# Performance work log

Hardware: AMD Instinct MI355X
Metric: run time of the kernel (lower is better)

Reference implementation:

```python
import jax, jax.numpy as jnp
import numpy as np

V, E, H, LE, B, T = 32001, 512, 512, 512, 128, 512
EPS = 1e-5


def setup_inputs() -> dict:
    key = jax.random.key(0)
    ks = jax.random.split(key, 12)
    s = 0.02
    return {
        "label": jax.random.randint(ks[0], (B, T), 0, V, dtype=jnp.int64) if jax.config.jax_enable_x64 else jax.random.randint(ks[0], (B, T), 0, V, dtype=jnp.int32),
        "label_len": jax.random.randint(ks[1], (B,), 0, T, dtype=jnp.int32),
        "embed_w": jax.random.normal(ks[2], (V, E), jnp.float32) * s,
        "i2h_w": jax.random.normal(ks[3], (5 * H, E), jnp.float32) * s,
        "i2h_b": jax.random.normal(ks[4], (5 * H,), jnp.float32) * s,
        "h2h_w": jax.random.normal(ks[5], (5 * H, H), jnp.float32) * s,
        "h2h_b": jax.random.normal(ks[6], (5 * H,), jnp.float32) * s,
        "lin0_w": jax.random.normal(ks[7], (LE, H), jnp.float32) * s,
        "lin0_b": jax.random.normal(ks[8], (LE,), jnp.float32) * s,
        "bn0_g": jnp.ones((LE,), jnp.float32),
        "bn0_b": jnp.zeros((LE,), jnp.float32),
        "lin1_w": jax.random.normal(ks[9], (LE, LE), jnp.float32) * s,
        "lin1_b": jax.random.normal(ks[10], (LE,), jnp.float32) * s,
        "bn1_g": jnp.ones((LE,), jnp.float32),
        "bn1_b": jnp.zeros((LE,), jnp.float32),
    }


def _batchnorm(x, g, b):
    # BatchNorm1d in training mode: biased batch statistics over batch dim
    m = jnp.mean(x, axis=0)
    v = jnp.mean((x - m) ** 2, axis=0)
    return (x - m) * jax.lax.rsqrt(v + EPS) * g + b


def reference(label, label_len, embed_w, i2h_w, i2h_b, h2h_w, h2h_b,
              lin0_w, lin0_b, bn0_g, bn0_b, lin1_w, lin1_b, bn1_g, bn1_b):
    xt = embed_w[label]                                   # [B,T,E]
    pre = jnp.einsum('bte,ge->btg', xt, i2h_w) + i2h_b    # precomputed i2h, [B,T,5H]
    pre = pre.transpose(1, 0, 2)                          # [T,B,5H]

    def step(carry, p_t):
        h, c = carry
        s = p_t + h @ h2h_w.T + h2h_b                     # [B,5H]
        sig = jax.nn.sigmoid(s[:, :3 * H])
        in_g, f_g, out_g = sig[:, :H], sig[:, H:2 * H], sig[:, 2 * H:3 * H]
        in_t = jnp.maximum(s[:, 3 * H:4 * H], s[:, 4 * H:5 * H])  # maxout transform
        nc = f_g * c + in_g * in_t
        nh = out_g * jnp.tanh(nc)
        return (nh, nc), nh

    h0 = jnp.zeros((B, H), pre.dtype)
    _, outs = jax.lax.scan(step, (h0, h0), pre)           # outs: [T,B,H]

    # pick output at timestep label_len[i] for each sample
    x = outs[label_len, jnp.arange(B)]                    # [B,H]

    x = _batchnorm(x @ lin0_w.T + lin0_b, bn0_g, bn0_b)
    x = jax.nn.relu(x)                                    # dropout identity (eval)
    x = _batchnorm(x @ lin1_w.T + lin1_b, bn1_g, bn1_b)
    return x
```

## Files before the change

kernel.cpp:

```cpp
#include <hip/hip_runtime.h>

typedef _Float16 h16x8 __attribute__((ext_vector_type(8)));
typedef _Float16 h16x4 __attribute__((ext_vector_type(4)));
typedef float fx4 __attribute__((ext_vector_type(4)));
typedef unsigned int u32x4 __attribute__((ext_vector_type(4)));
typedef unsigned long long ull;

#define PRE_S 2560.0f
#define PRE_INV (1.0f / 2560.0f)

__global__ __launch_bounds__(256) void f2h_kernel(const float* __restrict__ src,
                                                  _Float16* __restrict__ dst,
                                                  int n4) {
  int i = blockIdx.x * 256 + threadIdx.x;
  if (i < n4) {
    float4 v = ((const float4*)src)[i];
    h16x4 o = {(_Float16)v.x, (_Float16)v.y, (_Float16)v.z, (_Float16)v.w};
    *(h16x4*)&dst[i * 4] = o;
  }
}

__global__ __launch_bounds__(256) void gemm1_kernel(
    const int* __restrict__ label, const int* __restrict__ label_len,
    const float* __restrict__ embed_w,
    const _Float16* __restrict__ Bh,
    signed char* __restrict__ pre8) {
  const int bx = blockIdx.x;
  const int by = blockIdx.y;
  const int bidx = by >> 2;
  const int t0 = (by & 3) * 128;
  if (t0 > label_len[bidx]) return;

  const int tid = threadIdx.x;
  const int lane = tid & 63;
  const int wv = tid >> 6;
  const int wm = (wv & 1) * 64;
  const int wn = (wv >> 1) * 64;

  __shared__ _Float16 As[128 * 40];
  __shared__ _Float16 Bs[128 * 40];

  fx4 zero = {0.f, 0.f, 0.f, 0.f};
  fx4 acc[4][4];
  for (int a = 0; a < 4; a++)
    for (int b = 0; b < 4; b++) acc[a][b] = zero;

#pragma unroll 1
  for (int k0 = 0; k0 < 512; k0 += 32) {
#pragma unroll
    for (int q = 0; q < 2; q++) {
      int chunk = tid + q * 256;
      int row = chunk >> 2;
      int ko = (chunk & 3) * 8;
      int arow = label[bidx * 512 + t0 + row];
      const float* ap = &embed_w[(size_t)arow * 512 + k0 + ko];
      float4 a0 = *(const float4*)ap;
      float4 a1 = *(const float4*)(ap + 4);
      h16x8 av = {(_Float16)a0.x, (_Float16)a0.y, (_Float16)a0.z, (_Float16)a0.w,
                  (_Float16)a1.x, (_Float16)a1.y, (_Float16)a1.z, (_Float16)a1.w};
      h16x8 bv = *(const h16x8*)&Bh[(size_t)(bx * 128 + row) * 512 + k0 + ko];
      *(h16x8*)&As[row * 40 + ko] = av;
      *(h16x8*)&Bs[row * 40 + ko] = bv;
    }
    __syncthreads();
    h16x8 af[4], bfr[4];
#pragma unroll
    for (int i = 0; i < 4; i++) {
      af[i]  = *(const h16x8*)&As[(wm + i * 16 + (lane & 15)) * 40 + (lane >> 4) * 8];
      bfr[i] = *(const h16x8*)&Bs[(wn + i * 16 + (lane & 15)) * 40 + (lane >> 4) * 8];
    }
#pragma unroll
    for (int mi = 0; mi < 4; mi++)
#pragma unroll
      for (int ni = 0; ni < 4; ni++)
        acc[mi][ni] = __builtin_amdgcn_mfma_f32_16x16x32_f16(af[mi], bfr[ni], acc[mi][ni], 0, 0, 0);
    __syncthreads();
  }

#pragma unroll
  for (int mi = 0; mi < 4; mi++)
#pragma unroll
    for (int ni = 0; ni < 4; ni++)
#pragma unroll
      for (int r = 0; r < 4; r++) {
        int rowm = wm + mi * 16 + (lane >> 4) * 4 + r;
        int t = t0 + rowm;
        int n = bx * 128 + wn + ni * 16 + (lane & 15);
        float v = acc[mi][ni][r] * PRE_S;
        int q = (int)rintf(v);
        q = q > 127 ? 127 : (q < -127 ? -127 : q);
        int g = n >> 9, ju = n & 511, j = ju >> 3, u = ju & 7;
        pre8[(((size_t)t * 64 + j) * 128 + bidx) * 40 + g * 8 + u] = (signed char)q;
      }
}

#define NWG 128
__global__ __launch_bounds__(256, 1) void lstm_kernel(
    const int* __restrict__ label_len,
    const float* __restrict__ h2h_w,
    const float* __restrict__ h2h_b,
    const float* __restrict__ i2h_b,
    const signed char* __restrict__ pre8,
    _Float16* __restrict__ hfrag,
    float* __restrict__ xsel,
    int* __restrict__ flags) {
  const int j   = blockIdx.x >> 1;
  const int bh  = blockIdx.x & 1;
  const int tid = threadIdx.x;
  const int lane = tid & 63;
  const int wv = tid >> 6;

  __shared__ _Float16 Wl[3 * 16 * 64 * 8];
  __shared__ _Float16 s_s[64 * 48];
  __shared__ int ll_s[64];

  for (int slot = tid; slot < 3 * 16 * 64; slot += 256) {
    int nt = slot / (16 * 64);
    int rem = slot - nt * (16 * 64);
    int kt = rem >> 6;
    int l = rem & 63;
    int p = nt * 16 + (l & 15);
    int k0 = kt * 32 + (l >> 4) * 8;
    h16x8 tv;
    if (p < 40) {
      int r = (p >> 3) * 512 + j * 8 + (p & 7);
      const float* src = h2h_w + (size_t)r * 512 + k0;
#pragma unroll
      for (int q = 0; q < 8; q++) tv[q] = (_Float16)src[q];
    } else {
#pragma unroll
      for (int q = 0; q < 8; q++) tv[q] = (_Float16)0.f;
    }
    *(h16x8*)&Wl[slot * 8] = tv;
  }
  if (tid < 64) ll_s[tid] = label_len[bh * 64 + tid];

  const int ue = (tid & 3) * 2;
  const int bp = tid >> 2;
  float bias_r[2][5];
#pragma unroll
  for (int uu = 0; uu < 2; uu++)
#pragma unroll
    for (int g = 0; g < 5; g++)
      bias_r[uu][g] = h2h_b[g * 512 + j * 8 + ue + uu] + i2h_b[g * 512 + j * 8 + ue + uu];

  const int pbb = (bh * 4 + (bp >> 4)) * 16 + (j >> 2);
  const int plc = (bp & 15) | ((j & 3) << 4);
  unsigned int* pdst0 = (unsigned int*)(hfrag + (size_t)pbb * 512 + plc * 8 + ue);
  unsigned int* pdst1 = (unsigned int*)(hfrag + 65536 + (size_t)pbb * 512 + plc * 8 + ue);

  float c_reg[2] = {0.f, 0.f};
  __syncthreads();

#pragma unroll 1
  for (int t = 0; t < 512; ++t) {
    unsigned short pr[5];
    {
      const signed char* pt = pre8 + (((size_t)t * 64 + j) * 128 + bh * 64) * 40;
#pragma unroll
      for (int g = 0; g < 5; g++)
        pr[g] = *(const unsigned short*)&pt[bp * 40 + g * 8 + ue];
    }

    if (t > 0) {
      if (wv == 0) {
        const int* fp = flags + (bh * 64 + lane) * 32;
        while (true) {
          int v = __hip_atomic_load(fp, __ATOMIC_RELAXED, __HIP_MEMORY_SCOPE_AGENT);
          if (__ballot(v >= t) == 0xFFFFFFFFFFFFFFFFull) break;
          __builtin_amdgcn_s_sleep(1);
        }
      }
      __syncthreads();

      const _Float16* hpb = hfrag + ((t - 1) & 1) * 65536
                          + (size_t)((bh * 4 + wv) * 16) * 512 + lane * 8;
      u32x4 areg[16];
#pragma unroll
      for (int kt = 0; kt < 16; ++kt) {
        const void* ap = (const void*)(hpb + kt * 512);
        asm volatile("global_load_dwordx4 %0, %1, off sc0 sc1"
                     : "=v"(areg[kt]) : "v"(ap) : "memory");
      }
      asm volatile("s_waitcnt vmcnt(0)" ::: "memory");

      fx4 zero = {0.f, 0.f, 0.f, 0.f};
      fx4 acc[3] = {zero, zero, zero};
#pragma unroll
      for (int kt = 0; kt < 16; ++kt) {
        union { u32x4 u; h16x8 v; } a;
        a.u = areg[kt];
#pragma unroll
        for (int nt = 0; nt < 3; nt++) {
          h16x8 bfr = *(const h16x8*)&Wl[((nt * 16 + kt) * 64 + lane) * 8];
          acc[nt] = __builtin_amdgcn_mfma_f32_16x16x32_f16(a.v, bfr, acc[nt], 0, 0, 0);
        }
      }
#pragma unroll
      for (int nt = 0; nt < 3; nt++)
#pragma unroll
        for (int r = 0; r < 4; r++) {
          int b = wv * 16 + (lane >> 4) * 4 + r;
          s_s[b * 48 + nt * 16 + (lane & 15)] = (_Float16)acc[nt][r];
        }
      __syncthreads();
    }

    float nh2[2];
#pragma unroll
    for (int uu = 0; uu < 2; uu++) {
      float sv[5];
#pragma unroll
      for (int g = 0; g < 5; g++) {
        signed char qb = (signed char)(uu == 0 ? (pr[g] & 0xFF) : (pr[g] >> 8));
        float base = (t > 0) ? (float)s_s[bp * 48 + g * 8 + ue + uu] : 0.f;
        sv[g] = base + (float)qb * PRE_INV + bias_r[uu][g];
      }
      float ing = 1.f / (1.f + __expf(-sv[0]));
      float fg  = 1.f / (1.f + __expf(-sv[1]));
      float og  = 1.f / (1.f + __expf(-sv[2]));
      float itv = fmaxf(sv[3], sv[4]);
      float nc = fg * c_reg[uu] + ing * itv;
      c_reg[uu] = nc;
      nh2[uu] = og * tanhf(nc);
    }
    {
      union { _Float16 h[2]; unsigned int u; } pk;
      pk.h[0] = (_Float16)nh2[0];
      pk.h[1] = (_Float16)nh2[1];
      __hip_atomic_store((t & 1) ? pdst1 : pdst0, pk.u,
                         __ATOMIC_RELAXED, __HIP_MEMORY_SCOPE_AGENT);
      if (ll_s[bp] == t) {
        union { float f[2]; ull u; } xk;
        xk.f[0] = nh2[0];
        xk.f[1] = nh2[1];
        __hip_atomic_store((ull*)&xsel[(bh * 64 + bp) * 512 + j * 8 + ue], xk.u,
                           __ATOMIC_RELAXED, __HIP_MEMORY_SCOPE_AGENT);
      }
    }

    asm volatile("s_waitcnt vmcnt(0)" ::: "memory");
    __syncthreads();
    if (tid == 0)
      __hip_atomic_store(flags + (bh * 64 + j) * 32, t + 1,
                         __ATOMIC_RELAXED, __HIP_MEMORY_SCOPE_AGENT);
  }
}

__global__ __launch_bounds__(256) void fgemm_kernel(
    const float* __restrict__ X, const float* __restrict__ W,
    const float* __restrict__ bias, float* __restrict__ Y) {
  const int n0 = blockIdx.x * 64;
  const int m0 = blockIdx.y * 64;
  const int tid = threadIdx.x;
  const int tx = tid & 15, ty = tid >> 4;

  __shared__ float Xs[64 * 68];
  __shared__ float Wt[64 * 68];

  float acc[4][4] = {};
#pragma unroll 1
  for (int k0 = 0; k0 < 512; k0 += 64) {
#pragma unroll
    for (int q = 0; q < 4; q++) {
      int id = tid + q * 256;
      int r = id >> 4, c = id & 15;
      float4 xv = *(const float4*)&X[(m0 + r) * 512 + k0 + c * 4];
      *(float4*)&Xs[r * 68 + c * 4] = xv;
      float4 wvv = *(const float4*)&W[(n0 + r) * 512 + k0 + c * 4];
      Wt[(c * 4 + 0) * 68 + r] = wvv.x;
      Wt[(c * 4 + 1) * 68 + r] = wvv.y;
      Wt[(c * 4 + 2) * 68 + r] = wvv.z;
      Wt[(c * 4 + 3) * 68 + r] = wvv.w;
    }
    __syncthreads();
#pragma unroll 4
    for (int kk = 0; kk < 64; kk++) {
      float a[4], b[4];
#pragma unroll
      for (int i = 0; i < 4; i++) a[i] = Xs[(ty * 4 + i) * 68 + kk];
#pragma unroll
      for (int jj = 0; jj < 4; jj++) b[jj] = Wt[kk * 68 + tx * 4 + jj];
#pragma unroll
      for (int i = 0; i < 4; i++)
#pragma unroll
        for (int jj = 0; jj < 4; jj++) acc[i][jj] += a[i] * b[jj];
    }
    __syncthreads();
  }
#pragma unroll
  for (int i = 0; i < 4; i++)
#pragma unroll
    for (int jj = 0; jj < 4; jj++) {
      int n = n0 + tx * 4 + jj;
      Y[(m0 + ty * 4 + i) * 512 + n] = acc[i][jj] + bias[n];
    }
}

__global__ __launch_bounds__(256) void bn_kernel(float* __restrict__ Y,
    const float* __restrict__ gam, const float* __restrict__ bet, int relu) {
  const int cx = threadIdx.x & 15;
  const int rg = threadIdx.x >> 4;
  const int col = blockIdx.x * 16 + cx;
  __shared__ float rs[16 * 17], rs2[16 * 17];
  float s = 0.f, s2 = 0.f;
#pragma unroll
  for (int i = 0; i < 8; i++) {
    float v = Y[(rg * 8 + i) * 512 + col];
    s += v; s2 += v * v;
  }
  rs[rg * 17 + cx] = s;
  rs2[rg * 17 + cx] = s2;
  __syncthreads();
  if (threadIdx.x < 16) {
    float S = 0.f, S2 = 0.f;
#pragma unroll
    for (int q = 0; q < 16; q++) { S += rs[q * 17 + threadIdx.x]; S2 += rs2[q * 17 + threadIdx.x]; }
    float mean = S / 128.f;
    float var = S2 / 128.f - mean * mean;
    rs[threadIdx.x] = mean;
    rs2[threadIdx.x] = rsqrtf(var + 1e-5f);
  }
  __syncthreads();
  float mean = rs[cx], rstd = rs2[cx];
  float gv = gam[col], bv = bet[col];
#pragma unroll
  for (int i = 0; i < 8; i++) {
    int idx = (rg * 8 + i) * 512 + col;
    float v = (Y[idx] - mean) * rstd * gv + bv;
    if (relu) v = fmaxf(v, 0.f);
    Y[idx] = v;
  }
}

extern "C" void kernel_launch(void* const* d_in, const int* in_sizes, int n_in,
                              void* d_out, int out_size, void* d_ws, size_t ws_size,
                              hipStream_t stream) {
  const int* label      = (const int*)d_in[0];
  const int* label_len  = (const int*)d_in[1];
  const float* embed_w  = (const float*)d_in[2];
  const float* i2h_w    = (const float*)d_in[3];
  const float* i2h_b    = (const float*)d_in[4];
  const float* h2h_w    = (const float*)d_in[5];
  const float* h2h_b    = (const float*)d_in[6];
  const float* lin0_w   = (const float*)d_in[7];
  const float* lin0_b   = (const float*)d_in[8];
  const float* bn0_g    = (const float*)d_in[9];
  const float* bn0_b    = (const float*)d_in[10];
  const float* lin1_w   = (const float*)d_in[11];
  const float* lin1_b   = (const float*)d_in[12];
  const float* bn1_g    = (const float*)d_in[13];
  const float* bn1_b    = (const float*)d_in[14];
  float* out = (float*)d_out;
  char* ws = (char*)d_ws;

  const size_t OFF_FLAGS = 0;
  const size_t OFF_I2H  = 16384;
  const size_t OFF_PRE  = OFF_I2H + (size_t)2560 * 512 * 2;
  const size_t OFF_H    = OFF_PRE + (size_t)512 * 128 * 2560;
  const size_t OFF_XSEL = OFF_H + (size_t)2 * 128 * 512 * 2;
  const size_t OFF_Y0   = OFF_XSEL + (size_t)128 * 512 * 4;

  int* flags = (int*)(ws + OFF_FLAGS);
  _Float16* i2h_h = (_Float16*)(ws + OFF_I2H);
  signed char* pre8 = (signed char*)(ws + OFF_PRE);
  _Float16* hfrag = (_Float16*)(ws + OFF_H);
  float* xsel = (float*)(ws + OFF_XSEL);
  float* y0   = (float*)(ws + OFF_Y0);

  hipMemsetAsync(ws + OFF_FLAGS, 0, 16384, stream);

  {
    int n4 = (2560 * 512) / 4;
    f2h_kernel<<<(n4 + 255) / 256, 256, 0, stream>>>(i2h_w, i2h_h, n4);
  }
  gemm1_kernel<<<dim3(20, 512), 256, 0, stream>>>(label, label_len, embed_w, i2h_h, pre8);
  lstm_kernel<<<dim3(NWG), 256, 0, stream>>>(label_len, h2h_w, h2h_b, i2h_b, pre8, hfrag, xsel, flags);
  fgemm_kernel<<<dim3(8, 2), 256, 0, stream>>>(xsel, lin0_w, lin0_b, y0);
  bn_kernel<<<dim3(32), 256, 0, stream>>>(y0, bn0_g, bn0_b, 1);
  fgemm_kernel<<<dim3(8, 2), 256, 0, stream>>>(y0, lin1_w, lin1_b, out);
  bn_kernel<<<dim3(32), 256, 0, stream>>>(out, bn1_g, bn1_b, 0);
}
```

Before: 2.506 ms.

## Remap LSTM recurrence to 64 workgroups of 16 hidden units each

The recurrent kernel now gives each workgroup 16 hidden units instead of 8, so the five gate tiles fill the MFMA tiles without zero padding. Gate pre-activations now stay in registers instead of going through an LDS buffer. The quantized i2h tensor is laid out so that each lane reads its four batch rows with one dword load. The k-loop waits on the hidden-state loads in chunks so MFMAs can start before all loads land. The loop stops after the maximum label_len, and the activations use fast reciprocal and exp-based tanh. Each workgroup does more MFMA work per step, but there are half as many flags to poll and less LDS traffic, with some loss of accuracy in the nonlinearities.

```diff
diff --git a/kernel.cpp b/kernel.cpp
--- a/kernel.cpp
+++ b/kernel.cpp
@@ -89,12 +89,12 @@
         float v = acc[mi][ni][r] * PRE_S;
         int q = (int)rintf(v);
         q = q > 127 ? 127 : (q < -127 ? -127 : q);
-        int g = n >> 9, ju = n & 511, j = ju >> 3, u = ju & 7;
-        pre8[(((size_t)t * 64 + j) * 128 + bidx) * 40 + g * 8 + u] = (signed char)q;
-      }
-}
-
-#define NWG 128
+        int g = n >> 9, ju = n & 511, jj = ju >> 4, u = ju & 15;
+        pre8[((((size_t)t * 32 + jj) * 16 + u) * 5 + g) * 128 + bidx] = (signed char)q;
+      }
+}
+
+#define NWG 64
 __global__ __launch_bounds__(256, 1) void lstm_kernel(
     const int* __restrict__ label_len,
     const float* __restrict__ h2h_w,
@@ -104,69 +104,72 @@
     _Float16* __restrict__ hfrag,
     float* __restrict__ xsel,
     int* __restrict__ flags) {
-  const int j   = blockIdx.x >> 1;
+  const int jj  = blockIdx.x >> 1;
   const int bh  = blockIdx.x & 1;
   const int tid = threadIdx.x;
   const int lane = tid & 63;
   const int wv = tid >> 6;
 
-  __shared__ _Float16 Wl[3 * 16 * 64 * 8];
-  __shared__ _Float16 s_s[64 * 48];
+  __shared__ _Float16 Wl[5 * 16 * 64 * 8];
+  __shared__ _Float16 hstage[64 * 16];
   __shared__ int ll_s[64];
 
-  for (int slot = tid; slot < 3 * 16 * 64; slot += 256) {
-    int nt = slot / (16 * 64);
-    int rem = slot - nt * (16 * 64);
+  for (int slot = tid; slot < 5 * 16 * 64; slot += 256) {
+    int nt = slot >> 10;
+    int rem = slot & 1023;
     int kt = rem >> 6;
     int l = rem & 63;
-    int p = nt * 16 + (l & 15);
+    int r = nt * 512 + jj * 16 + (l & 15);
     int k0 = kt * 32 + (l >> 4) * 8;
+    const float* src = h2h_w + (size_t)r * 512 + k0;
     h16x8 tv;
-    if (p < 40) {
-      int r = (p >> 3) * 512 + j * 8 + (p & 7);
-      const float* src = h2h_w + (size_t)r * 512 + k0;
-#pragma unroll
-      for (int q = 0; q < 8; q++) tv[q] = (_Float16)src[q];
-    } else {
-#pragma unroll
-      for (int q = 0; q < 8; q++) tv[q] = (_Float16)0.f;
-    }
+#pragma unroll
+    for (int q = 0; q < 8; q++) tv[q] = (_Float16)src[q];
     *(h16x8*)&Wl[slot * 8] = tv;
   }
   if (tid < 64) ll_s[tid] = label_len[bh * 64 + tid];
-
-  const int ue = (tid & 3) * 2;
+  __syncthreads();
+
+  int tmax = 0;
+#pragma unroll 1
+  for (int i = 0; i < 64; i++) tmax = max(tmax, ll_s[i]);
+  tmax += 1;
+
+  const int u = lane & 15;
+  const int b4 = wv * 16 + (lane >> 4) * 4;
+  float bias_r[5];
+#pragma unroll
+  for (int g = 0; g < 5; g++)
+    bias_r[g] = h2h_b[g * 512 + jj * 16 + u] + i2h_b[g * 512 + jj * 16 + u];
+
   const int bp = tid >> 2;
-  float bias_r[2][5];
-#pragma unroll
-  for (int uu = 0; uu < 2; uu++)
-#pragma unroll
-    for (int g = 0; g < 5; g++)
-      bias_r[uu][g] = h2h_b[g * 512 + j * 8 + ue + uu] + i2h_b[g * 512 + j * 8 + ue + uu];
-
-  const int pbb = (bh * 4 + (bp >> 4)) * 16 + (j >> 2);
-  const int plc = (bp & 15) | ((j & 3) << 4);
-  unsigned int* pdst0 = (unsigned int*)(hfrag + (size_t)pbb * 512 + plc * 8 + ue);
-  unsigned int* pdst1 = (unsigned int*)(hfrag + 65536 + (size_t)pbb * 512 + plc * 8 + ue);
-
-  float c_reg[2] = {0.f, 0.f};
-  __syncthreads();
+  const int ue = (tid & 3) * 4;
+  const int pbb = (bh * 4 + (bp >> 4)) * 16 + (jj >> 1);
+  const int pl2 = (bp & 15) | ((2 * (jj & 1) + (ue >> 3)) << 4);
+  ull* pdst0 = (ull*)(hfrag + (size_t)pbb * 512 + pl2 * 8 + (ue & 4));
+  ull* pdst1 = (ull*)(hfrag + 65536 + (size_t)pbb * 512 + pl2 * 8 + (ue & 4));
+
+  const int* pollp = flags + (bh * 32 + (lane & 31)) * 32;
+  const int myflag = (bh * 32 + jj) * 32;
+
+  float c_reg[4] = {0.f, 0.f, 0.f, 0.f};
 
 #pragma unroll 1
-  for (int t = 0; t < 512; ++t) {
-    unsigned short pr[5];
+  for (int t = 0; t < tmax; ++t) {
+    unsigned int pr[5];
     {
-      const signed char* pt = pre8 + (((size_t)t * 64 + j) * 128 + bh * 64) * 40;
+      const signed char* pt = pre8 + ((((size_t)t * 32 + jj) * 16 + u) * 5) * 128
+                            + bh * 64 + b4;
 #pragma unroll
       for (int g = 0; g < 5; g++)
-        pr[g] = *(const unsigned short*)&pt[bp * 40 + g * 8 + ue];
-    }
-
+        pr[g] = *(const unsigned int*)(pt + g * 128);
+    }
+
+    fx4 acc[5] = {};
     if (t > 0) {
       if (wv == 0) {
-        const int* fp = flags + (bh * 64 + lane) * 32;
         while (true) {
-          int v = __hip_atomic_load(fp, __ATOMIC_RELAXED, __HIP_MEMORY_SCOPE_AGENT);
+          int v = __hip_atomic_load(pollp, __ATOMIC_RELAXED, __HIP_MEMORY_SCOPE_AGENT);
           if (__ballot(v >= t) == 0xFFFFFFFFFFFFFFFFull) break;
           __builtin_amdgcn_s_sleep(1);
         }
@@ -182,67 +185,59 @@
         asm volatile("global_load_dwordx4 %0, %1, off sc0 sc1"
                      : "=v"(areg[kt]) : "v"(ap) : "memory");
       }
-      asm volatile("s_waitcnt vmcnt(0)" ::: "memory");
-
-      fx4 zero = {0.f, 0.f, 0.f, 0.f};
-      fx4 acc[3] = {zero, zero, zero};
-#pragma unroll
-      for (int kt = 0; kt < 16; ++kt) {
-        union { u32x4 u; h16x8 v; } a;
-        a.u = areg[kt];
-#pragma unroll
-        for (int nt = 0; nt < 3; nt++) {
-          h16x8 bfr = *(const h16x8*)&Wl[((nt * 16 + kt) * 64 + lane) * 8];
-          acc[nt] = __builtin_amdgcn_mfma_f32_16x16x32_f16(a.v, bfr, acc[nt], 0, 0, 0);
-        }
-      }
-#pragma unroll
-      for (int nt = 0; nt < 3; nt++)
-#pragma unroll
-        for (int r = 0; r < 4; r++) {
-          int b = wv * 16 + (lane >> 4) * 4 + r;
-          s_s[b * 48 + nt * 16 + (lane & 15)] = (_Float16)acc[nt][r];
-        }
-      __syncthreads();
-    }
-
-    float nh2[2];
-#pragma unroll
-    for (int uu = 0; uu < 2; uu++) {
+
+#define GCHUNK(K0, VCSTR)                                                        \
+      asm volatile("s_waitcnt vmcnt(" VCSTR ")" ::: "memory");                   \
+      __builtin_amdgcn_sched_barrier(0);                                         \
+      _Pragma("unroll")                                                          \
+      for (int kt = (K0); kt < (K0) + 4; ++kt) {                                 \
+        union { u32x4 uu; h16x8 v; } aa;                                         \
+        aa.uu = areg[kt];                                                        \
+        _Pragma("unroll")                                                        \
+        for (int nt = 0; nt < 5; nt++) {                                         \
+          h16x8 bfr = *(const h16x8*)&Wl[((nt * 16 + kt) * 64 + lane) * 8];      \
+          acc[nt] = __builtin_amdgcn_mfma_f32_16x16x32_f16(aa.v, bfr, acc[nt], 0, 0, 0); \
+        }                                                                        \
+      }
+      GCHUNK(0, "12")
+      GCHUNK(4, "8")
+      GCHUNK(8, "4")
+      GCHUNK(12, "0")
+#undef GCHUNK
+    }
+
+#pragma unroll
+    for (int r = 0; r < 4; r++) {
       float sv[5];
 #pragma unroll
       for (int g = 0; g < 5; g++) {
-        signed char qb = (signed char)(uu == 0 ? (pr[g] & 0xFF) : (pr[g] >> 8));
-        float base = (t > 0) ? (float)s_s[bp * 48 + g * 8 + ue + uu] : 0.f;
-        sv[g] = base + (float)qb * PRE_INV + bias_r[uu][g];
-      }
-      float ing = 1.f / (1.f + __expf(-sv[0]));
-      float fg  = 1.f / (1.f + __expf(-sv[1]));
-      float og  = 1.f / (1.f + __expf(-sv[2]));
+        signed char qb = (signed char)((pr[g] >> (8 * r)) & 0xFF);
+        sv[g] = acc[g][r] + (float)qb * PRE_INV + bias_r[g];
+      }
+      float ing = __builtin_amdgcn_rcpf(1.f + __expf(-sv[0]));
+      float fg  = __builtin_amdgcn_rcpf(1.f + __expf(-sv[1]));
+      float og  = __builtin_amdgcn_rcpf(1.f + __expf(-sv[2]));
       float itv = fmaxf(sv[3], sv[4]);
-      float nc = fg * c_reg[uu] + ing * itv;
-      c_reg[uu] = nc;
-      nh2[uu] = og * tanhf(nc);
-    }
+      float nc  = fg * c_reg[r] + ing * itv;
+      c_reg[r] = nc;
+      float nh = og * (1.f - 2.f * __builtin_amdgcn_rcpf(__expf(2.f * nc) + 1.f));
+      hstage[(b4 + r) * 16 + u] = (_Float16)nh;
+      if (ll_s[b4 + r] == t)
+        xsel[(bh * 64 + b4 + r) * 512 + jj * 16 + u] = nh;
+    }
+    __syncthreads();
+
     {
-      union { _Float16 h[2]; unsigned int u; } pk;
-      pk.h[0] = (_Float16)nh2[0];
-      pk.h[1] = (_Float16)nh2[1];
-      __hip_atomic_store((t & 1) ? pdst1 : pdst0, pk.u,
+      union { h16x4 h4; ull u8; } pk;
+      pk.h4 = *(const h16x4*)&hstage[bp * 16 + ue];
+      __hip_atomic_store((t & 1) ? pdst1 : pdst0, pk.u8,
                          __ATOMIC_RELAXED, __HIP_MEMORY_SCOPE_AGENT);
-      if (ll_s[bp] == t) {
-        union { float f[2]; ull u; } xk;
-        xk.f[0] = nh2[0];
-        xk.f[1] = nh2[1];
-        __hip_atomic_store((ull*)&xsel[(bh * 64 + bp) * 512 + j * 8 + ue], xk.u,
-                           __ATOMIC_RELAXED, __HIP_MEMORY_SCOPE_AGENT);
-      }
     }
 
     asm volatile("s_waitcnt vmcnt(0)" ::: "memory");
     __syncthreads();
     if (tid == 0)
-      __hip_atomic_store(flags + (bh * 64 + j) * 32, t + 1,
+      __hip_atomic_store(flags + myflag, t + 1,
                          __ATOMIC_RELAXED, __HIP_MEMORY_SCOPE_AGENT);
   }
 }
```

Result: slower. 3.373 ms (+34.6%).
